# Kernel tuning notes

Hardware: AMD Instinct MI355X
Metric: run time of the kernel (lower is better)

The kernel has to match this reference:

```python
import jax, jax.numpy as jnp
import numpy as np


def setup_inputs() -> dict:
    key = jax.random.key(0)
    kq, kk, kv = jax.random.split(key, 3)
    B, S, D = 8, 2048, 128
    Q = jax.random.normal(kq, (B, S, D), dtype=jnp.float32)
    K = jax.random.normal(kk, (B, S, D), dtype=jnp.float32)
    V = jax.random.normal(kv, (B, S, D), dtype=jnp.float32)
    return {"Q": Q, "K": K, "V": V}


def reference(Q, K, V):
    # scores: [B, S, S]
    d = Q.shape[-1]
    scores = jnp.einsum('bqd,bkd->bqk', Q, K) / jnp.sqrt(jnp.float32(d))
    # causal mask: position i attends to keys <= i (original sets upper triangle to -inf)
    S = scores.shape[-1]
    causal = jnp.tril(jnp.ones((S, S), dtype=bool))  # [S, S]
    scores = jnp.where(causal[None, :, :], scores, -jnp.inf)
    probs = jax.nn.softmax(scores, axis=-1)
    return jnp.einsum('bqk,bkd->bqd', probs, V)
```

## Files before the change

### kernel.cpp

```cpp
#include <hip/hip_runtime.h>

#define BB 8
#define SS 2048
#define DD 128

typedef _Float16 f16;
typedef _Float16 f16x8 __attribute__((ext_vector_type(8)));
typedef float f32x4 __attribute__((ext_vector_type(4)));

static __device__ __forceinline__ unsigned short f2h(float x) {
    f16 h = (f16)x;
    return __builtin_bit_cast(unsigned short, h);
}

static __device__ __forceinline__ float fast_exp2(float x) {
#if __has_builtin(__builtin_amdgcn_exp2f)
    return __builtin_amdgcn_exp2f(x);
#else
    return exp2f(x);
#endif
}

template <bool SPLIT>
__global__ __launch_bounds__(256, 2)
void attn_fwd(const float* __restrict__ Qg, const float* __restrict__ Kg,
              const float* __restrict__ Vg, float* __restrict__ Og,
              float* __restrict__ O1, float2* __restrict__ ml0,
              float2* __restrict__ ml1)
{
    __shared__ __align__(16) f16 Kl[64 * 128];
    __shared__ __align__(16) f16 Vt[128 * 64];
    __shared__ __align__(16) f16 Pl[4][16 * 64];

    const int tid  = threadIdx.x;
    const int lane = tid & 63;
    const int w    = tid >> 6;
    const int c_   = lane & 15;
    const int g    = lane >> 4;

    const int L  = blockIdx.x;
    const int bb = L & 7;
    int qb, hv, t0, t1;
    if (SPLIT) {
        const int rem = L >> 3;
        qb = 31 - (rem >> 1);
        hv = rem & 1;
        const int T   = qb + 1;
        const int Th0 = (T + 1) >> 1;
        t0 = hv ? Th0 : 0;
        t1 = hv ? T : Th0;
    } else {
        qb = 31 - (L >> 3);
        hv = 0;
        t0 = 0;
        t1 = qb + 1;
    }

    const int qrow0 = qb * 64 + w * 16;

    const float qs = 0.08838834764831845f * 1.4426950408889634f;
    f16x8 qf[4];
    {
        const float* qp = Qg + (size_t)(bb * SS + qrow0 + c_) * DD;
#pragma unroll
        for (int kk = 0; kk < 4; ++kk) {
            const int d0 = kk * 32 + g * 8;
            f32x4 a = *(const f32x4*)(qp + d0);
            f32x4 b = *(const f32x4*)(qp + d0 + 4);
            f16x8 q;
#pragma unroll
            for (int i = 0; i < 4; ++i) {
                q[i]     = (f16)(a[i] * qs);
                q[i + 4] = (f16)(b[i] * qs);
            }
            qf[kk] = q;
        }
    }

    f32x4 Oa[8];
#pragma unroll
    for (int i = 0; i < 8; ++i) Oa[i] = (f32x4){0.f, 0.f, 0.f, 0.f};
    float mrun[4] = {-1e30f, -1e30f, -1e30f, -1e30f};
    float lrun[4] = {0.f, 0.f, 0.f, 0.f};

    f16* Pw = &Pl[w][0];

    const int krow = tid >> 5;
    const int kc4  = tid & 31;
    const int vkg  = tid >> 5;
    const int vq   = tid & 31;

    f32x4 kreg[8], vreg[8];

    if (t0 < t1) {
        {
            const size_t gb = (size_t)(bb * SS + t0 * 64) * DD;
#pragma unroll
            for (int j = 0; j < 8; ++j)
                kreg[j] = *(const f32x4*)(Kg + gb + (krow + 8 * j) * DD + kc4 * 4);
#pragma unroll
            for (int i = 0; i < 8; ++i)
                vreg[i] = *(const f32x4*)(Vg + gb + (vkg * 8 + i) * DD + vq * 4);
        }

        for (int t = t0; t < t1; ++t) {
            __syncthreads();
#pragma unroll
            for (int j = 0; j < 8; ++j) {
                const int row = krow + 8 * j;
                const int el  = row * 128 + ((kc4 * 4) ^ ((row & 7) << 3));
                f32x4 v = kreg[j];
                ushort4 u;
                u.x = f2h(v[0]); u.y = f2h(v[1]); u.z = f2h(v[2]); u.w = f2h(v[3]);
                *(ushort4*)&Kl[el] = u;
            }
#pragma unroll
            for (int dd = 0; dd < 4; ++dd) {
                const int d  = vq * 4 + dd;
                const int sw = (d & 7) << 3;
#pragma unroll
                for (int h = 0; h < 2; ++h) {
                    ushort4 u;
                    u.x = f2h(vreg[4 * h + 0][dd]);
                    u.y = f2h(vreg[4 * h + 1][dd]);
                    u.z = f2h(vreg[4 * h + 2][dd]);
                    u.w = f2h(vreg[4 * h + 3][dd]);
                    const int el = d * 64 + ((vkg * 8 + 4 * h) ^ sw);
                    *(ushort4*)&Vt[el] = u;
                }
            }
            __syncthreads();

            if (t + 1 < t1) {
                const size_t gb = (size_t)(bb * SS + (t + 1) * 64) * DD;
#pragma unroll
                for (int j = 0; j < 8; ++j)
                    kreg[j] = *(const f32x4*)(Kg + gb + (krow + 8 * j) * DD + kc4 * 4);
#pragma unroll
                for (int i = 0; i < 8; ++i)
                    vreg[i] = *(const f32x4*)(Vg + gb + (vkg * 8 + i) * DD + vq * 4);
            }

            const int kbase = t * 64;

            f32x4 s[4];
#pragma unroll
            for (int nb = 0; nb < 4; ++nb) {
                f32x4 acc = (f32x4){0.f, 0.f, 0.f, 0.f};
                const int row = c_ + nb * 16;
                const int sw  = (row & 7) << 3;
#pragma unroll
                for (int kk = 0; kk < 4; ++kk) {
                    f16x8 kb = *(const f16x8*)&Kl[row * 128 + ((kk * 32 + g * 8) ^ sw)];
                    acc = __builtin_amdgcn_mfma_f32_16x16x32_f16(qf[kk], kb, acc, 0, 0, 0);
                }
                s[nb] = acc;
            }

            if (t == qb) {
#pragma unroll
                for (int nb = 0; nb < 4; ++nb)
#pragma unroll
                    for (int r = 0; r < 4; ++r) {
                        const int kj = kbase + nb * 16 + c_;
                        const int qi = qrow0 + g * 4 + r;
                        if (kj > qi) s[nb][r] = -1e30f;
                    }
            }

            float pm[4], sc[4];
#pragma unroll
            for (int r = 0; r < 4; ++r) {
                float v = fmaxf(fmaxf(s[0][r], s[1][r]), fmaxf(s[2][r], s[3][r]));
                v = fmaxf(v, __shfl_xor(v, 1));
                v = fmaxf(v, __shfl_xor(v, 2));
                v = fmaxf(v, __shfl_xor(v, 4));
                v = fmaxf(v, __shfl_xor(v, 8));
                pm[r] = v;
            }
#pragma unroll
            for (int r = 0; r < 4; ++r) {
                float mn = fmaxf(mrun[r], pm[r]);
                sc[r]   = fast_exp2(mrun[r] - mn);
                mrun[r] = mn;
            }
            float rs[4] = {0.f, 0.f, 0.f, 0.f};
            f16 pv16[4][4];
#pragma unroll
            for (int nb = 0; nb < 4; ++nb)
#pragma unroll
                for (int r = 0; r < 4; ++r) {
                    float pv = fast_exp2(s[nb][r] - mrun[r]);
                    rs[r] += pv;
                    pv16[nb][r] = (f16)pv;
                }
#pragma unroll
            for (int r = 0; r < 4; ++r) {
                float v = rs[r];
                v += __shfl_xor(v, 1);
                v += __shfl_xor(v, 2);
                v += __shfl_xor(v, 4);
                v += __shfl_xor(v, 8);
                lrun[r] = lrun[r] * sc[r] + v;
            }
#pragma unroll
            for (int dblk = 0; dblk < 8; ++dblk)
#pragma unroll
                for (int r = 0; r < 4; ++r) Oa[dblk][r] *= sc[r];

#pragma unroll
            for (int nb = 0; nb < 4; ++nb)
#pragma unroll
                for (int r = 0; r < 4; ++r) {
                    const int row = g * 4 + r;
                    Pw[row * 64 + ((nb * 16 + c_) ^ ((row & 7) << 3))] = pv16[nb][r];
                }

#pragma unroll
            for (int ks = 0; ks < 2; ++ks) {
                f16x8 pa = *(const f16x8*)&Pw[c_ * 64 + ((ks * 32 + g * 8) ^ ((c_ & 7) << 3))];
#pragma unroll
                for (int dblk = 0; dblk < 8; ++dblk) {
                    const int d  = dblk * 16 + c_;
                    f16x8 vb = *(const f16x8*)&Vt[d * 64 + ((ks * 32 + g * 8) ^ ((d & 7) << 3))];
                    Oa[dblk] = __builtin_amdgcn_mfma_f32_16x16x32_f16(pa, vb, Oa[dblk], 0, 0, 0);
                }
            }
        }
    }

    if (SPLIT) {
        float*  od  = hv ? O1 : Og;
        float2* mld = hv ? ml1 : ml0;
#pragma unroll
        for (int r = 0; r < 4; ++r) {
            const int qrow = qrow0 + g * 4 + r;
            float* dst = od + (size_t)(bb * SS + qrow) * DD + c_;
#pragma unroll
            for (int dblk = 0; dblk < 8; ++dblk) dst[dblk * 16] = Oa[dblk][r];
            if (c_ == 0) mld[bb * SS + qrow] = make_float2(mrun[r], lrun[r]);
        }
    } else {
#pragma unroll
        for (int r = 0; r < 4; ++r) {
            const int qrow = qrow0 + g * 4 + r;
            float* dst = Og + (size_t)(bb * SS + qrow) * DD + c_;
            const float inv = 1.0f / lrun[r];
#pragma unroll
            for (int dblk = 0; dblk < 8; ++dblk) dst[dblk * 16] = Oa[dblk][r] * inv;
        }
    }
}

__global__ __launch_bounds__(256)
void merge_kernel(float* __restrict__ out, const float* __restrict__ O1,
                  const float2* __restrict__ ml0, const float2* __restrict__ ml1)
{
    const int idx = blockIdx.x * 256 + threadIdx.x;
    const int row = idx >> 5;
    const float2 a = ml0[row];
    const float2 b = ml1[row];
    const float mm = fmaxf(a.x, b.x);
    const float e0 = fast_exp2(a.x - mm);
    const float e1 = fast_exp2(b.x - mm);
    const float inv = 1.0f / (a.y * e0 + b.y * e1);
    float4 o0 = ((const float4*)out)[idx];
    float4 o1 = ((const float4*)O1)[idx];
    float4 r;
    r.x = (o0.x * e0 + o1.x * e1) * inv;
    r.y = (o0.y * e0 + o1.y * e1) * inv;
    r.z = (o0.z * e0 + o1.z * e1) * inv;
    r.w = (o0.w * e0 + o1.w * e1) * inv;
    ((float4*)out)[idx] = r;
}

extern "C" void kernel_launch(void* const* d_in, const int* in_sizes, int n_in,
                              void* d_out, int out_size, void* d_ws, size_t ws_size,
                              hipStream_t stream)
{
    const float* Q = (const float*)d_in[0];
    const float* K = (const float*)d_in[1];
    const float* V = (const float*)d_in[2];
    float* out = (float*)d_out;

    const size_t O1_bytes = (size_t)BB * SS * DD * sizeof(float);
    const size_t ml_bytes = (size_t)BB * SS * sizeof(float2);
    const size_t need     = O1_bytes + 2 * ml_bytes;

    if (ws_size >= need) {
        float*  O1  = (float*)d_ws;
        float2* ml0 = (float2*)((char*)d_ws + O1_bytes);
        float2* ml1 = ml0 + (size_t)BB * SS;
        hipLaunchKernelGGL((attn_fwd<true>), dim3(512), dim3(256), 0, stream,
                           Q, K, V, out, O1, ml0, ml1);
        hipLaunchKernelGGL(merge_kernel, dim3(BB * SS * DD / 4 / 256), dim3(256),
                           0, stream, out, O1, ml0, ml1);
    } else {
        hipLaunchKernelGGL((attn_fwd<false>), dim3(256), dim3(256), 0, stream,
                           Q, K, V, out, (float*)nullptr,
                           (float2*)nullptr, (float2*)nullptr);
    }
}
```

Measured before the change: 116.4 us.

## Generalize KV split to four ways with lazy rescaling, setprio, and V swizzle

Generalizes the flash-decoding style KV split from two to NS partitions (four when workspace allows) and templates the merge kernel to match, adding parallelism for the short causal rows. It also adds a lazy max update that skips the O rescale when the new max exceeds the old by at most 8, and defers the row-sum shuffle reduction to the end of the loop. Separately it wraps the MFMA blocks in s_setprio and uses a stronger XOR swizzle on the transposed V tile to cut LDS bank conflicts. The costs are more partial-output traffic (three extra O buffers) and a heavier merge pass.

```diff
diff --git a/kernel.cpp b/kernel.cpp
--- a/kernel.cpp
+++ b/kernel.cpp
@@ -7,6 +7,8 @@
 typedef _Float16 f16;
 typedef _Float16 f16x8 __attribute__((ext_vector_type(8)));
 typedef float f32x4 __attribute__((ext_vector_type(4)));
+
+#define SWV(d) ((((d) & 7) ^ (((d) >> 3) & 7)) << 3)
 
 static __device__ __forceinline__ unsigned short f2h(float x) {
     f16 h = (f16)x;
@@ -21,12 +23,11 @@
 #endif
 }
 
-template <bool SPLIT>
+template <int NS>
 __global__ __launch_bounds__(256, 2)
 void attn_fwd(const float* __restrict__ Qg, const float* __restrict__ Kg,
               const float* __restrict__ Vg, float* __restrict__ Og,
-              float* __restrict__ O1, float2* __restrict__ ml0,
-              float2* __restrict__ ml1)
+              float* __restrict__ Opart, float2* __restrict__ mlb)
 {
     __shared__ __align__(16) f16 Kl[64 * 128];
     __shared__ __align__(16) f16 Vt[128 * 64];
@@ -38,23 +39,14 @@
     const int c_   = lane & 15;
     const int g    = lane >> 4;
 
-    const int L  = blockIdx.x;
-    const int bb = L & 7;
-    int qb, hv, t0, t1;
-    if (SPLIT) {
-        const int rem = L >> 3;
-        qb = 31 - (rem >> 1);
-        hv = rem & 1;
-        const int T   = qb + 1;
-        const int Th0 = (T + 1) >> 1;
-        t0 = hv ? Th0 : 0;
-        t1 = hv ? T : Th0;
-    } else {
-        qb = 31 - (L >> 3);
-        hv = 0;
-        t0 = 0;
-        t1 = qb + 1;
-    }
+    const int L   = blockIdx.x;
+    const int bb  = L & 7;
+    const int rem = L >> 3;
+    const int qb  = 31 - (rem / NS);
+    const int s   = rem % NS;
+    const int T   = qb + 1;
+    const int t0  = (T * s) / NS;
+    const int t1  = (T * (s + 1)) / NS;
 
     const int qrow0 = qb * 64 + w * 16;
 
@@ -81,7 +73,7 @@
 #pragma unroll
     for (int i = 0; i < 8; ++i) Oa[i] = (f32x4){0.f, 0.f, 0.f, 0.f};
     float mrun[4] = {-1e30f, -1e30f, -1e30f, -1e30f};
-    float lrun[4] = {0.f, 0.f, 0.f, 0.f};
+    float lpart[4] = {0.f, 0.f, 0.f, 0.f};
 
     f16* Pw = &Pl[w][0];
 
@@ -117,7 +109,7 @@
 #pragma unroll
             for (int dd = 0; dd < 4; ++dd) {
                 const int d  = vq * 4 + dd;
-                const int sw = (d & 7) << 3;
+                const int sw = SWV(d);
 #pragma unroll
                 for (int h = 0; h < 2; ++h) {
                     ushort4 u;
@@ -143,7 +135,8 @@
 
             const int kbase = t * 64;
 
-            f32x4 s[4];
+            f32x4 s4[4];
+            __builtin_amdgcn_s_setprio(1);
 #pragma unroll
             for (int nb = 0; nb < 4; ++nb) {
                 f32x4 acc = (f32x4){0.f, 0.f, 0.f, 0.f};
@@ -154,8 +147,9 @@
                     f16x8 kb = *(const f16x8*)&Kl[row * 128 + ((kk * 32 + g * 8) ^ sw)];
                     acc = __builtin_amdgcn_mfma_f32_16x16x32_f16(qf[kk], kb, acc, 0, 0, 0);
                 }
-                s[nb] = acc;
-            }
+                s4[nb] = acc;
+            }
+            __builtin_amdgcn_s_setprio(0);
 
             if (t == qb) {
 #pragma unroll
@@ -164,14 +158,14 @@
                     for (int r = 0; r < 4; ++r) {
                         const int kj = kbase + nb * 16 + c_;
                         const int qi = qrow0 + g * 4 + r;
-                        if (kj > qi) s[nb][r] = -1e30f;
+                        if (kj > qi) s4[nb][r] = -1e30f;
                     }
             }
 
             float pm[4], sc[4];
 #pragma unroll
             for (int r = 0; r < 4; ++r) {
-                float v = fmaxf(fmaxf(s[0][r], s[1][r]), fmaxf(s[2][r], s[3][r]));
+                float v = fmaxf(fmaxf(s4[0][r], s4[1][r]), fmaxf(s4[2][r], s4[3][r]));
                 v = fmaxf(v, __shfl_xor(v, 1));
                 v = fmaxf(v, __shfl_xor(v, 2));
                 v = fmaxf(v, __shfl_xor(v, 4));
@@ -180,8 +174,9 @@
             }
 #pragma unroll
             for (int r = 0; r < 4; ++r) {
-                float mn = fmaxf(mrun[r], pm[r]);
-                sc[r]   = fast_exp2(mrun[r] - mn);
+                const bool keep = (pm[r] - mrun[r] <= 8.0f);
+                const float mn  = keep ? mrun[r] : pm[r];
+                sc[r]   = keep ? 1.0f : fast_exp2(mrun[r] - pm[r]);
                 mrun[r] = mn;
             }
             float rs[4] = {0.f, 0.f, 0.f, 0.f};
@@ -190,23 +185,19 @@
             for (int nb = 0; nb < 4; ++nb)
 #pragma unroll
                 for (int r = 0; r < 4; ++r) {
-                    float pv = fast_exp2(s[nb][r] - mrun[r]);
+                    float pv = fast_exp2(s4[nb][r] - mrun[r]);
                     rs[r] += pv;
                     pv16[nb][r] = (f16)pv;
                 }
-#pragma unroll
-            for (int r = 0; r < 4; ++r) {
-                float v = rs[r];
-                v += __shfl_xor(v, 1);
-                v += __shfl_xor(v, 2);
-                v += __shfl_xor(v, 4);
-                v += __shfl_xor(v, 8);
-                lrun[r] = lrun[r] * sc[r] + v;
-            }
-#pragma unroll
-            for (int dblk = 0; dblk < 8; ++dblk)
-#pragma unroll
-                for (int r = 0; r < 4; ++r) Oa[dblk][r] *= sc[r];
+            const float scmin = fminf(fminf(sc[0], sc[1]), fminf(sc[2], sc[3]));
+            if (scmin < 1.0f) {
+#pragma unroll
+                for (int dblk = 0; dblk < 8; ++dblk)
+#pragma unroll
+                    for (int r = 0; r < 4; ++r) Oa[dblk][r] *= sc[r];
+            }
+#pragma unroll
+            for (int r = 0; r < 4; ++r) lpart[r] = lpart[r] * sc[r] + rs[r];
 
 #pragma unroll
             for (int nb = 0; nb < 4; ++nb)
@@ -219,28 +210,30 @@
 #pragma unroll
             for (int ks = 0; ks < 2; ++ks) {
                 f16x8 pa = *(const f16x8*)&Pw[c_ * 64 + ((ks * 32 + g * 8) ^ ((c_ & 7) << 3))];
+                __builtin_amdgcn_s_setprio(1);
 #pragma unroll
                 for (int dblk = 0; dblk < 8; ++dblk) {
                     const int d  = dblk * 16 + c_;
-                    f16x8 vb = *(const f16x8*)&Vt[d * 64 + ((ks * 32 + g * 8) ^ ((d & 7) << 3))];
+                    f16x8 vb = *(const f16x8*)&Vt[d * 64 + ((ks * 32 + g * 8) ^ SWV(d))];
                     Oa[dblk] = __builtin_amdgcn_mfma_f32_16x16x32_f16(pa, vb, Oa[dblk], 0, 0, 0);
                 }
-            }
-        }
-    }
-
-    if (SPLIT) {
-        float*  od  = hv ? O1 : Og;
-        float2* mld = hv ? ml1 : ml0;
-#pragma unroll
-        for (int r = 0; r < 4; ++r) {
-            const int qrow = qrow0 + g * 4 + r;
-            float* dst = od + (size_t)(bb * SS + qrow) * DD + c_;
-#pragma unroll
-            for (int dblk = 0; dblk < 8; ++dblk) dst[dblk * 16] = Oa[dblk][r];
-            if (c_ == 0) mld[bb * SS + qrow] = make_float2(mrun[r], lrun[r]);
-        }
-    } else {
+                __builtin_amdgcn_s_setprio(0);
+            }
+        }
+    }
+
+    float lrun[4];
+#pragma unroll
+    for (int r = 0; r < 4; ++r) {
+        float v = lpart[r];
+        v += __shfl_xor(v, 1);
+        v += __shfl_xor(v, 2);
+        v += __shfl_xor(v, 4);
+        v += __shfl_xor(v, 8);
+        lrun[r] = v;
+    }
+
+    if (NS == 1) {
 #pragma unroll
         for (int r = 0; r < 4; ++r) {
             const int qrow = qrow0 + g * 4 + r;
@@ -249,29 +242,52 @@
 #pragma unroll
             for (int dblk = 0; dblk < 8; ++dblk) dst[dblk * 16] = Oa[dblk][r] * inv;
         }
-    }
-}
-
+    } else {
+        float*  od  = (s == 0) ? Og : (Opart + (size_t)(s - 1) * BB * SS * DD);
+        float2* mld = mlb + (size_t)s * BB * SS;
+#pragma unroll
+        for (int r = 0; r < 4; ++r) {
+            const int qrow = qrow0 + g * 4 + r;
+            float* dst = od + (size_t)(bb * SS + qrow) * DD + c_;
+#pragma unroll
+            for (int dblk = 0; dblk < 8; ++dblk) dst[dblk * 16] = Oa[dblk][r];
+            if (c_ == 0) mld[bb * SS + qrow] = make_float2(mrun[r], lrun[r]);
+        }
+    }
+}
+
+template <int NS>
 __global__ __launch_bounds__(256)
-void merge_kernel(float* __restrict__ out, const float* __restrict__ O1,
-                  const float2* __restrict__ ml0, const float2* __restrict__ ml1)
+void merge_kernel(float* __restrict__ out, const float* __restrict__ Opart,
+                  const float2* __restrict__ mlb)
 {
     const int idx = blockIdx.x * 256 + threadIdx.x;
     const int row = idx >> 5;
-    const float2 a = ml0[row];
-    const float2 b = ml1[row];
-    const float mm = fmaxf(a.x, b.x);
-    const float e0 = fast_exp2(a.x - mm);
-    const float e1 = fast_exp2(b.x - mm);
-    const float inv = 1.0f / (a.y * e0 + b.y * e1);
-    float4 o0 = ((const float4*)out)[idx];
-    float4 o1 = ((const float4*)O1)[idx];
-    float4 r;
-    r.x = (o0.x * e0 + o1.x * e1) * inv;
-    r.y = (o0.y * e0 + o1.y * e1) * inv;
-    r.z = (o0.z * e0 + o1.z * e1) * inv;
-    r.w = (o0.w * e0 + o1.w * e1) * inv;
-    ((float4*)out)[idx] = r;
+    float2 ml[NS];
+#pragma unroll
+    for (int i = 0; i < NS; ++i) ml[i] = mlb[(size_t)i * BB * SS + row];
+    float mm = ml[0].x;
+#pragma unroll
+    for (int i = 1; i < NS; ++i) mm = fmaxf(mm, ml[i].x);
+    float e[NS], den = 0.f;
+#pragma unroll
+    for (int i = 0; i < NS; ++i) {
+        e[i] = fast_exp2(ml[i].x - mm);
+        den += ml[i].y * e[i];
+    }
+    const float inv = 1.0f / den;
+    float4 o = ((const float4*)out)[idx];
+    float4 acc;
+    acc.x = o.x * e[0]; acc.y = o.y * e[0];
+    acc.z = o.z * e[0]; acc.w = o.w * e[0];
+#pragma unroll
+    for (int i = 1; i < NS; ++i) {
+        float4 p = ((const float4*)(Opart + (size_t)(i - 1) * BB * SS * DD))[idx];
+        acc.x += p.x * e[i]; acc.y += p.y * e[i];
+        acc.z += p.z * e[i]; acc.w += p.w * e[i];
+    }
+    acc.x *= inv; acc.y *= inv; acc.z *= inv; acc.w *= inv;
+    ((float4*)out)[idx] = acc;
 }
 
 extern "C" void kernel_launch(void* const* d_in, const int* in_sizes, int n_in,
@@ -283,21 +299,29 @@
     const float* V = (const float*)d_in[2];
     float* out = (float*)d_out;
 
-    const size_t O1_bytes = (size_t)BB * SS * DD * sizeof(float);
-    const size_t ml_bytes = (size_t)BB * SS * sizeof(float2);
-    const size_t need     = O1_bytes + 2 * ml_bytes;
-
-    if (ws_size >= need) {
-        float*  O1  = (float*)d_ws;
-        float2* ml0 = (float2*)((char*)d_ws + O1_bytes);
-        float2* ml1 = ml0 + (size_t)BB * SS;
-        hipLaunchKernelGGL((attn_fwd<true>), dim3(512), dim3(256), 0, stream,
-                           Q, K, V, out, O1, ml0, ml1);
-        hipLaunchKernelGGL(merge_kernel, dim3(BB * SS * DD / 4 / 256), dim3(256),
-                           0, stream, out, O1, ml0, ml1);
+    const size_t OB = (size_t)BB * SS * DD * sizeof(float);
+    const size_t MB_ = (size_t)BB * SS * sizeof(float2);
+    const int mergeGrid = BB * SS * DD / 4 / 256;
+
+    const size_t need4 = 3 * OB + 4 * MB_;
+    const size_t need2 = 1 * OB + 2 * MB_;
+
+    if (ws_size >= need4) {
+        float*  Op  = (float*)d_ws;
+        float2* mlb = (float2*)((char*)d_ws + 3 * OB);
+        hipLaunchKernelGGL((attn_fwd<4>), dim3(8 * 32 * 4), dim3(256), 0, stream,
+                           Q, K, V, out, Op, mlb);
+        hipLaunchKernelGGL((merge_kernel<4>), dim3(mergeGrid), dim3(256), 0, stream,
+                           out, Op, mlb);
+    } else if (ws_size >= need2) {
+        float*  Op  = (float*)d_ws;
+        float2* mlb = (float2*)((char*)d_ws + 1 * OB);
+        hipLaunchKernelGGL((attn_fwd<2>), dim3(8 * 32 * 2), dim3(256), 0, stream,
+                           Q, K, V, out, Op, mlb);
+        hipLaunchKernelGGL((merge_kernel<2>), dim3(mergeGrid), dim3(256), 0, stream,
+                           out, Op, mlb);
     } else {
-        hipLaunchKernelGGL((attn_fwd<false>), dim3(256), dim3(256), 0, stream,
-                           Q, K, V, out, (float*)nullptr,
-                           (float2*)nullptr, (float2*)nullptr);
-    }
-}
+        hipLaunchKernelGGL((attn_fwd<1>), dim3(8 * 32), dim3(256), 0, stream,
+                           Q, K, V, out, (float*)nullptr, (float2*)nullptr);
+    }
+}
```

Result: faster. 105.7 us (-9.2%).
